# Kernel tuning notes

Hardware: AMD Instinct MI355X
Metric: run time of the kernel (lower is better)

The kernel has to match this reference:

```python
import jax, jax.numpy as jnp
import numpy as np

D_MODEL = 1024
NUM_HEADS = 16
HEAD_DIM = D_MODEL // NUM_HEADS


def setup_inputs() -> dict:
    key = jax.random.key(0)
    ks = jax.random.split(key, 5)
    x = jax.random.normal(ks[0], (2, 2048, D_MODEL), dtype=jnp.float32)
    s = 1.0 / np.sqrt(D_MODEL)
    # nn.Linear weight is [out, in]; y = x @ W.T
    Wq = jax.random.normal(ks[1], (D_MODEL, D_MODEL), dtype=jnp.float32) * s
    Wk = jax.random.normal(ks[2], (D_MODEL, D_MODEL), dtype=jnp.float32) * s
    Wv = jax.random.normal(ks[3], (D_MODEL, D_MODEL), dtype=jnp.float32) * s
    Wo = jax.random.normal(ks[4], (D_MODEL, D_MODEL), dtype=jnp.float32) * s
    return {"x": x, "Wq": Wq, "Wk": Wk, "Wv": Wv, "Wo": Wo}


def reference(x, Wq, Wk, Wv, Wo):
    b, s, d = x.shape
    h, hd = NUM_HEADS, HEAD_DIM
    # projections (Linear: x @ W.T), reshape to [b, h, s, hd]
    def proj(W):
        return (x @ W.T).reshape(b, s, h, hd).transpose(0, 2, 1, 3)
    Q, K, V = proj(Wq), proj(Wk), proj(Wv)
    # NOTE: original scales by 1/sqrt(d_model), not 1/sqrt(head_dim)
    scores = jnp.einsum('bhqd,bhkd->bhqk', Q, K) / jnp.sqrt(jnp.float32(d))
    attn = jax.nn.softmax(scores, axis=-1)
    ctx = jnp.einsum('bhqk,bhkd->bhqd', attn, V)
    ctx = ctx.transpose(0, 2, 1, 3).reshape(b, s, d)
    return ctx @ Wo.T
```

## Files before the change

kernel.cpp:

```cpp
#include <hip/hip_runtime.h>
#include <cstddef>
#include <cstdint>

#define SEQ 2048
#define DM 1024
#define NH 16
#define HD 64

typedef _Float16 f16;
typedef __attribute__((ext_vector_type(8))) _Float16 f16x8;
typedef __attribute__((ext_vector_type(4))) _Float16 f16x4;
typedef __attribute__((ext_vector_type(2))) _Float16 f16x2;
typedef __attribute__((ext_vector_type(4))) float f32x4;

__global__ __launch_bounds__(256) void cast_all(const float* __restrict__ x,
                                                const float* __restrict__ Wq,
                                                const float* __restrict__ Wk,
                                                const float* __restrict__ Wv,
                                                const float* __restrict__ Wo,
                                                f16* __restrict__ dst) {
  const int i = blockIdx.x * 256 + threadIdx.x;
  const float* src;
  int off;
  if (i < 1048576) {
    src = x; off = i;
  } else {
    const int j = i - 1048576;
    const int wsel = j >> 18;
    src = (wsel == 0) ? Wq : (wsel == 1) ? Wk : (wsel == 2) ? Wv : Wo;
    off = j & 262143;
  }
  const float4 v = ((const float4*)src)[off];
  f16x4 o = {(f16)v.x, (f16)v.y, (f16)v.z, (f16)v.w};
  ((f16x4*)dst)[i] = o;
}

__device__ __forceinline__ void gload16(const void* g, void* lds) {
  __builtin_amdgcn_global_load_lds((const __attribute__((address_space(1))) void*)g,
                                   (__attribute__((address_space(3))) void*)lds,
                                   16, 0, 0);
}

__device__ __forceinline__ void gemm_tile_db(const f16* __restrict__ A,
                                             const f16* __restrict__ B,
                                             f16* As0, f16* Bs0,
                                             f16* As1, f16* Bs1,
                                             int K, f32x4 acc[4][4]) {
  const int t = threadIdx.x, lane = t & 63, w = t >> 6;
  const int wm = (w & 1) << 6, wn = (w >> 1) << 6;
  const int srow = lane >> 3, sg = lane & 7;
  const int fr = lane & 15, q = lane >> 4;
  const int scol = (sg ^ srow) << 3;
  auto stg = [&](int k0, f16* As, f16* Bs) {
#pragma unroll
    for (int c = 0; c < 4; ++c) {
      const int row = (w << 5) + (c << 3) + srow;
      gload16(A + (size_t)row * K + k0 + scol, As + (w << 11) + (c << 9));
      gload16(B + (size_t)row * K + k0 + scol, Bs + (w << 11) + (c << 9));
    }
  };
  auto comp = [&](const f16* As, const f16* Bs) {
    f16x8 af[4][2], bf[4][2];
#pragma unroll
    for (int i = 0; i < 4; ++i) {
      const int row = wm + (i << 4) + fr;
#pragma unroll
      for (int kh = 0; kh < 2; ++kh)
        af[i][kh] = *(const f16x8*)(As + row * 64 +
                                    ((((kh << 2) | q) ^ (row & 7)) << 3));
    }
#pragma unroll
    for (int j = 0; j < 4; ++j) {
      const int row = wn + (j << 4) + fr;
#pragma unroll
      for (int kh = 0; kh < 2; ++kh)
        bf[j][kh] = *(const f16x8*)(Bs + row * 64 +
                                    ((((kh << 2) | q) ^ (row & 7)) << 3));
    }
#pragma unroll
    for (int kh = 0; kh < 2; ++kh)
#pragma unroll
      for (int i = 0; i < 4; ++i)
#pragma unroll
        for (int j = 0; j < 4; ++j)
          acc[i][j] = __builtin_amdgcn_mfma_f32_16x16x32_f16(af[i][kh], bf[j][kh],
                                                             acc[i][j], 0, 0, 0);
  };
  stg(0, As0, Bs0);
  for (int k0 = 0; k0 < K; k0 += 128) {
    __syncthreads();
    stg(k0 + 64, As1, Bs1);
    comp(As0, Bs0);
    __syncthreads();
    if (k0 + 128 < K) stg(k0 + 128, As0, Bs0);
    comp(As1, Bs1);
  }
}

#define QSCALE 0.04508422003f
__global__ __launch_bounds__(256) void gemm_qkv(
    const f16* __restrict__ xb, const f16* __restrict__ Wqb,
    const f16* __restrict__ Wkb, const f16* __restrict__ Wvb,
    f16* __restrict__ Qb, f16* __restrict__ Kb, f16* __restrict__ Vtg) {
  __shared__ f16 smem[32768];
  f16* As0 = smem;
  f16* Bs0 = smem + 8192;
  f16* As1 = smem + 16384;
  f16* Bs1 = smem + 24576;
  const int which = blockIdx.x >> 3;
  const int bn = (blockIdx.x & 7) << 7;
  const int bm = blockIdx.y << 7;
  const f16* B = (which == 0) ? Wqb : (which == 1) ? Wkb : Wvb;
  f32x4 acc[4][4] = {};
  gemm_tile_db(xb + (size_t)bm * DM, B + (size_t)bn * DM, As0, Bs0, As1, Bs1,
               DM, acc);
  const int lane = threadIdx.x & 63, w = threadIdx.x >> 6;
  const int wm = (w & 1) << 6, wn = (w >> 1) << 6;
  const int col = lane & 15, q = lane >> 4;
  if (which < 2) {
    f16* C = (which == 0) ? Qb : Kb;
    const float sc = (which == 0) ? QSCALE : 1.0f;
#pragma unroll
    for (int i = 0; i < 4; ++i) {
      const int m = bm + wm + (i << 4) + (q << 2);
#pragma unroll
      for (int j = 0; j < 4; ++j) {
        const int n = bn + wn + (j << 4) + col;
#pragma unroll
        for (int r = 0; r < 4; ++r)
          C[(size_t)(m + r) * DM + n] = (f16)(acc[i][j][r] * sc);
      }
    }
  } else {
    __syncthreads();
#pragma unroll
    for (int i = 0; i < 4; ++i) {
      const int m0 = wm + (i << 4) + (q << 2);
      const int cm = m0 >> 3, sub = (m0 >> 2) & 1;
#pragma unroll
      for (int j = 0; j < 4; ++j) {
        const int nl = wn + (j << 4) + col;
        f16x4 o = {(f16)acc[i][j][0], (f16)acc[i][j][1],
                   (f16)acc[i][j][2], (f16)acc[i][j][3]};
        *(f16x4*)(smem + nl * 128 +
                  ((cm ^ (nl & 15) ^ ((nl >> 4) & 3)) << 3) + (sub << 2)) = o;
      }
    }
    __syncthreads();
    const int b = bm >> 11, sb = bm & 2047;
    const int d = threadIdx.x & 63;
#pragma unroll
    for (int pr = 0; pr < 8; ++pr) {
      const int idx0 = (threadIdx.x >> 6) + (pr << 3);
      const int hh = idx0 >> 5;
      const int s40 = idx0 & 31;
      const int s41 = s40 + 4;
      const int nl = (hh << 6) + d;
      f16x4 va, vb;
      {
        const int cm = s40 >> 1, sub = s40 & 1;
        va = *(const f16x4*)(smem + nl * 128 +
                             ((cm ^ (nl & 15) ^ ((nl >> 4) & 3)) << 3) + (sub << 2));
      }
      {
        const int cm = s41 >> 1, sub = s41 & 1;
        vb = *(const f16x4*)(smem + nl * 128 +
                             ((cm ^ (nl & 15) ^ ((nl >> 4) & 3)) << 3) + (sub << 2));
      }
      const int bh = (b << 4) + (bn >> 6) + hh;
      const int kt = (sb >> 6) + (s40 >> 4);
      const int kc2 = (s40 & 15) >> 3, qd = s40 & 3;
      const f16x8 vv = __builtin_shufflevector(va, vb, 0, 1, 2, 3, 4, 5, 6, 7);
      const size_t flat = ((size_t)bh << 17) + ((size_t)kt << 12) +
                          ((size_t)kc2 << 11) + ((size_t)qd << 9) + ((size_t)d << 3);
      *(f16x8*)(Vtg + flat) = vv;
    }
  }
}

__global__ __launch_bounds__(256) void gemm_out(const f16* __restrict__ Ab,
                                                const f16* __restrict__ Wob,
                                                float* __restrict__ out) {
  __shared__ f16 smem[24576];
  f16* As0 = smem;
  f16* As1 = smem + 8192;
  f16* Bs0 = smem + 16384;
  f16* Bs1 = smem + 20480;
  const int bn = blockIdx.x << 6, bm = blockIdx.y << 7;
  const int t = threadIdx.x, lane = t & 63, w = t >> 6;
  const int srow = lane >> 3, sg = lane & 7;
  const int fr = lane & 15, q = lane >> 4;
  const int scol = (sg ^ srow) << 3;
  const f16* A = Ab + (size_t)bm * DM;
  const f16* B = Wob + (size_t)bn * DM;
  const int wm = w << 5;
  f32x4 acc[2][4] = {};
  auto stg = [&](int k0, f16* As, f16* Bs) {
#pragma unroll
    for (int c = 0; c < 4; ++c) {
      const int row = (w << 5) + (c << 3) + srow;
      gload16(A + (size_t)row * DM + k0 + scol, As + (w << 11) + (c << 9));
    }
#pragma unroll
    for (int c = 0; c < 2; ++c) {
      const int row = (w << 4) + (c << 3) + srow;
      gload16(B + (size_t)row * DM + k0 + scol, Bs + (w << 10) + (c << 9));
    }
  };
  auto comp = [&](const f16* As, const f16* Bs) {
    f16x8 af[2][2], bf[4][2];
#pragma unroll
    for (int i = 0; i < 2; ++i) {
      const int row = wm + (i << 4) + fr;
#pragma unroll
      for (int kh = 0; kh < 2; ++kh)
        af[i][kh] = *(const f16x8*)(As + row * 64 +
                                    ((((kh << 2) | q) ^ (row & 7)) << 3));
    }
#pragma unroll
    for (int j = 0; j < 4; ++j) {
      const int row = (j << 4) + fr;
#pragma unroll
      for (int kh = 0; kh < 2; ++kh)
        bf[j][kh] = *(const f16x8*)(Bs + row * 64 +
                                    ((((kh << 2) | q) ^ (row & 7)) << 3));
    }
#pragma unroll
    for (int kh = 0; kh < 2; ++kh)
#pragma unroll
      for (int i = 0; i < 2; ++i)
#pragma unroll
        for (int j = 0; j < 4; ++j)
          acc[i][j] = __builtin_amdgcn_mfma_f32_16x16x32_f16(af[i][kh], bf[j][kh],
                                                             acc[i][j], 0, 0, 0);
  };
  stg(0, As0, Bs0);
  for (int k0 = 0; k0 < DM; k0 += 128) {
    __syncthreads();
    stg(k0 + 64, As1, Bs1);
    comp(As0, Bs0);
    __syncthreads();
    if (k0 + 128 < DM) stg(k0 + 128, As0, Bs0);
    comp(As1, Bs1);
  }
  const int col = lane & 15;
#pragma unroll
  for (int i = 0; i < 2; ++i) {
    const int m = bm + wm + (i << 4) + (q << 2);
#pragma unroll
    for (int j = 0; j < 4; ++j) {
      const int n = bn + (j << 4) + col;
#pragma unroll
      for (int r = 0; r < 4; ++r)
        out[(size_t)(m + r) * DM + n] = acc[i][j][r];
    }
  }
}

__global__ __launch_bounds__(256, 2) void attn_mfma(const f16* __restrict__ Qb,
                                                    const f16* __restrict__ Kb,
                                                    const f16* __restrict__ Vtg,
                                                    f16* __restrict__ Ctx) {
  __shared__ f16 smem[16384];
  const int t = threadIdx.x, lane = t & 63, w = t >> 6;
  const int fr = lane & 15, quad = lane >> 4;
  const int i = blockIdx.x;
  const int j = i >> 3;
  const int bh = ((i & 7) << 2) + (j >> 4);
  const int qt16 = j & 15;
  const int b = bh >> 4, h = bh & 15;

  const size_t qrow0 = (size_t)b * SEQ + qt16 * 128 + w * 32;

  f16x8 Qf[2][2];
#pragma unroll
  for (int qt = 0; qt < 2; ++qt)
#pragma unroll
    for (int hf = 0; hf < 2; ++hf)
      Qf[qt][hf] = *(const f16x8*)(Qb + (qrow0 + qt * 16 + fr) * DM + h * HD +
                                   hf * 32 + (quad << 3));

  const int krow = lane >> 2;
  const int kkc = ((lane & 3) - (lane >> 3)) & 3;
  const f16* Kg = Kb + ((size_t)b * SEQ + 16 * w + krow) * DM + h * HD + (kkc << 3);
  const f16* Vg = Vtg + ((size_t)bh << 17) + (((w << 7) + lane) << 3);

  const int crd = ((fr >> 1) << 3) | ((fr & 1) << 2) | (((fr >> 1) + quad) & 3);

  f16* K0 = smem;
  f16* K1 = smem + 4096;
  f16* V0 = smem + 8192;
  f16* V1 = smem + 12288;

  auto stage = [&](int kt, f16* Kimg, f16* Vimg) {
#pragma unroll
    for (int hf = 0; hf < 2; ++hf)
      gload16(Kg + (size_t)kt * 64 * DM + hf * 32, Kimg + (hf << 11) + (w << 9));
#pragma unroll
    for (int c = 0; c < 2; ++c)
      gload16(Vg + kt * 4096 + (c << 9), Vimg + (w << 10) + (c << 9));
  };

  f32x4 acc[2][4] = {};
  float lacc[2] = {0.f, 0.f};
  f16x8 Kf[4][2];
  f16x8 VfA[4][2], pfA[2][2];
  f16x8 VfB[4][2], pfB[2][2];

  auto frags = [&](const f16* KR, const f16* VR, f16x8 (&Vf)[4][2]) {
#pragma unroll
    for (int mt = 0; mt < 4; ++mt)
#pragma unroll
      for (int hf = 0; hf < 2; ++hf)
        Kf[mt][hf] = *(const f16x8*)(KR + (crd << 3) + (hf << 11) + (mt << 9));
#pragma unroll
    for (int dt = 0; dt < 4; ++dt)
#pragma unroll
      for (int kc = 0; kc < 2; ++kc)
        Vf[dt][kc] = *(const f16x8*)(VR + (kc << 11) + (quad << 9) +
                                     (((dt << 4) | fr) << 3));
  };

  auto qkexp = [&](f16x8 (&pf)[2][2]) {
    f32x4 z[2][4] = {};
    __builtin_amdgcn_s_setprio(1);
#pragma unroll
    for (int hf = 0; hf < 2; ++hf)
#pragma unroll
      for (int qt = 0; qt < 2; ++qt)
#pragma unroll
        for (int mt = 0; mt < 4; ++mt)
          z[qt][mt] = __builtin_amdgcn_mfma_f32_16x16x32_f16(Kf[mt][hf], Qf[qt][hf],
                                                             z[qt][mt], 0, 0, 0);
    __builtin_amdgcn_s_setprio(0);
#pragma unroll
    for (int qt = 0; qt < 2; ++qt) {
      f16x4 p4[4];
#pragma unroll
      for (int mt = 0; mt < 4; ++mt) {
        const float p0 = __builtin_amdgcn_exp2f(z[qt][mt][0]);
        const float p1 = __builtin_amdgcn_exp2f(z[qt][mt][1]);
        const float p2 = __builtin_amdgcn_exp2f(z[qt][mt][2]);
        const float p3 = __builtin_amdgcn_exp2f(z[qt][mt][3]);
        lacc[qt] += (p0 + p1) + (p2 + p3);
        const f16x2 lo = __builtin_bit_cast(f16x2, __builtin_amdgcn_cvt_pkrtz(p0, p1));
        const f16x2 hi = __builtin_bit_cast(f16x2, __builtin_amdgcn_cvt_pkrtz(p2, p3));
        f16x4 pv4; pv4.x = lo.x; pv4.y = lo.y; pv4.z = hi.x; pv4.w = hi.y;
        p4[mt] = pv4;
      }
      pf[qt][0] = __builtin_shufflevector(p4[0], p4[1], 0, 1, 2, 3, 4, 5, 6, 7);
      pf[qt][1] = __builtin_shufflevector(p4[2], p4[3], 0, 1, 2, 3, 4, 5, 6, 7);
    }
  };

  auto pv = [&](const f16x8 (&Vf)[4][2], const f16x8 (&pf)[2][2]) {
    __builtin_amdgcn_s_setprio(1);
#pragma unroll
    for (int kc = 0; kc < 2; ++kc)
#pragma unroll
      for (int dt = 0; dt < 4; ++dt)
#pragma unroll
        for (int qt = 0; qt < 2; ++qt)
          acc[qt][dt] = __builtin_amdgcn_mfma_f32_16x16x32_f16(Vf[dt][kc], pf[qt][kc],
                                                               acc[qt][dt], 0, 0, 0);
    __builtin_amdgcn_s_setprio(0);
  };

  stage(0, K0, V0);

  __syncthreads();
  stage(1, K1, V1);
  frags(K0, V0, VfA);
  qkexp(pfA);
  __syncthreads();
  stage(2, K0, V0);
  frags(K1, V1, VfB);
  qkexp(pfB);

  for (int kt = 2; kt < 30; kt += 2) {
    __syncthreads();
    stage(kt + 1, K1, V1);
    pv(VfA, pfA);
    frags(K0, V0, VfA);
    qkexp(pfA);
    __syncthreads();
    stage(kt + 2, K0, V0);
    pv(VfB, pfB);
    frags(K1, V1, VfB);
    qkexp(pfB);
  }

  __syncthreads();
  stage(31, K1, V1);
  pv(VfA, pfA);
  frags(K0, V0, VfA);
  qkexp(pfA);
  __syncthreads();
  pv(VfB, pfB);
  frags(K1, V1, VfB);
  qkexp(pfB);
  pv(VfA, pfA);
  pv(VfB, pfB);

  float inv[2];
#pragma unroll
  for (int qt = 0; qt < 2; ++qt) {
    float l = lacc[qt];
    l += __shfl_xor(l, 16);
    l += __shfl_xor(l, 32);
    inv[qt] = __builtin_amdgcn_rcpf(l);
  }

  __syncthreads();
  f16* T = smem + (w << 11);
#pragma unroll
  for (int qt = 0; qt < 2; ++qt)
#pragma unroll
    for (int dt = 0; dt < 4; ++dt) {
      f16x4 o = {(f16)(acc[qt][dt][0] * inv[qt]), (f16)(acc[qt][dt][1] * inv[qt]),
                 (f16)(acc[qt][dt][2] * inv[qt]), (f16)(acc[qt][dt][3] * inv[qt])};
      *(f16x4*)(T + (qt * 16 + fr) * 64 + dt * 16 + (quad << 2)) = o;
    }
#pragma unroll
  for (int p = 0; p < 4; ++p) {
    const int ql = p * 8 + (lane >> 3);
    const f16x8 v = *(const f16x8*)(T + ql * 64 + ((lane & 7) << 3));
    *(f16x8*)(Ctx + (qrow0 + ql) * DM + h * HD + ((lane & 7) << 3)) = v;
  }
}

extern "C" void kernel_launch(void* const* d_in, const int* in_sizes, int n_in,
                              void* d_out, int out_size, void* d_ws, size_t ws_size,
                              hipStream_t stream) {
  const float* x  = (const float*)d_in[0];
  const float* Wq = (const float*)d_in[1];
  const float* Wk = (const float*)d_in[2];
  const float* Wv = (const float*)d_in[3];
  const float* Wo = (const float*)d_in[4];

  char* ws = (char*)d_ws;
  f16* xb  = (f16*)(ws);
  f16* Wb  = (f16*)(ws + (8u << 20));
  f16* Wqb = Wb;
  f16* Wkb = Wb + 1048576;
  f16* Wvb = Wb + 2097152;
  f16* Wob = Wb + 3145728;
  f16* Qb  = (f16*)(ws + (16u << 20));
  f16* Kb  = (f16*)(ws + (24u << 20));
  f16* Vtg = (f16*)(ws + (32u << 20));
  f16* Ctx = (f16*)(ws + (40u << 20));

  cast_all<<<8192, 256, 0, stream>>>(x, Wq, Wk, Wv, Wo, xb);

  gemm_qkv<<<dim3(24, 32), 256, 0, stream>>>(xb, Wqb, Wkb, Wvb, Qb, Kb, Vtg);
  attn_mfma<<<dim3(2 * NH * (SEQ / 128)), 256, 0, stream>>>(Qb, Kb, Vtg, Ctx);
  gemm_out<<<dim3(16, 32), 256, 0, stream>>>(Ctx, Wob, (float*)d_out);
}
```

Measured before the change: 164.6 us.

## Enlarge QKV projection GEMM tile to 256x256 with 512-thread blocks

```diff
diff --git a/kernel.cpp b/kernel.cpp
--- a/kernel.cpp
+++ b/kernel.cpp
@@ -41,91 +41,82 @@
                                    16, 0, 0);
 }
 
-__device__ __forceinline__ void gemm_tile_db(const f16* __restrict__ A,
-                                             const f16* __restrict__ B,
-                                             f16* As0, f16* Bs0,
-                                             f16* As1, f16* Bs1,
-                                             int K, f32x4 acc[4][4]) {
+#define QSCALE 0.04508422003f
+__global__ __launch_bounds__(512) void gemm_qkv(
+    const f16* __restrict__ xb, const f16* __restrict__ Wqb,
+    const f16* __restrict__ Wkb, const f16* __restrict__ Wvb,
+    f16* __restrict__ Qb, f16* __restrict__ Kb, f16* __restrict__ Vtg) {
+  __shared__ f16 smem[65536];
+  f16* As0 = smem;
+  f16* Bs0 = smem + 16384;
+  f16* As1 = smem + 32768;
+  f16* Bs1 = smem + 49152;
+  const int which = blockIdx.x >> 2;
+  const int bn = blockIdx.x & 3;
+  const int bm = blockIdx.y;
+  const f16* B = (which == 0) ? Wqb : (which == 1) ? Wkb : Wvb;
+  const f16* A = xb + ((size_t)bm << 8) * DM;
+  const f16* Bt = B + ((size_t)bn << 8) * DM;
+
   const int t = threadIdx.x, lane = t & 63, w = t >> 6;
-  const int wm = (w & 1) << 6, wn = (w >> 1) << 6;
+  const int wm = (w & 1) << 7, wn = (w >> 1) << 6;
   const int srow = lane >> 3, sg = lane & 7;
   const int fr = lane & 15, q = lane >> 4;
   const int scol = (sg ^ srow) << 3;
+
+  f32x4 acc[8][4] = {};
+
   auto stg = [&](int k0, f16* As, f16* Bs) {
 #pragma unroll
     for (int c = 0; c < 4; ++c) {
       const int row = (w << 5) + (c << 3) + srow;
-      gload16(A + (size_t)row * K + k0 + scol, As + (w << 11) + (c << 9));
-      gload16(B + (size_t)row * K + k0 + scol, Bs + (w << 11) + (c << 9));
+      gload16(A + (size_t)row * DM + k0 + scol, As + (w << 11) + (c << 9));
+      gload16(Bt + (size_t)row * DM + k0 + scol, Bs + (w << 11) + (c << 9));
     }
   };
   auto comp = [&](const f16* As, const f16* Bs) {
-    f16x8 af[4][2], bf[4][2];
-#pragma unroll
-    for (int i = 0; i < 4; ++i) {
-      const int row = wm + (i << 4) + fr;
-#pragma unroll
-      for (int kh = 0; kh < 2; ++kh)
-        af[i][kh] = *(const f16x8*)(As + row * 64 +
-                                    ((((kh << 2) | q) ^ (row & 7)) << 3));
-    }
-#pragma unroll
-    for (int j = 0; j < 4; ++j) {
-      const int row = wn + (j << 4) + fr;
-#pragma unroll
-      for (int kh = 0; kh < 2; ++kh)
-        bf[j][kh] = *(const f16x8*)(Bs + row * 64 +
-                                    ((((kh << 2) | q) ^ (row & 7)) << 3));
-    }
-#pragma unroll
-    for (int kh = 0; kh < 2; ++kh)
-#pragma unroll
-      for (int i = 0; i < 4; ++i)
+#pragma unroll
+    for (int kh = 0; kh < 2; ++kh) {
+      f16x8 bfk[4];
+#pragma unroll
+      for (int j = 0; j < 4; ++j) {
+        const int rowb = wn + (j << 4) + fr;
+        bfk[j] = *(const f16x8*)(Bs + rowb * 64 +
+                                 ((((kh << 2) | q) ^ (rowb & 7)) << 3));
+      }
+#pragma unroll
+      for (int i = 0; i < 8; ++i) {
+        const int rowa = wm + (i << 4) + fr;
+        const f16x8 a = *(const f16x8*)(As + rowa * 64 +
+                                        ((((kh << 2) | q) ^ (rowa & 7)) << 3));
 #pragma unroll
         for (int j = 0; j < 4; ++j)
-          acc[i][j] = __builtin_amdgcn_mfma_f32_16x16x32_f16(af[i][kh], bf[j][kh],
+          acc[i][j] = __builtin_amdgcn_mfma_f32_16x16x32_f16(a, bfk[j],
                                                              acc[i][j], 0, 0, 0);
-  };
+      }
+    }
+  };
+
   stg(0, As0, Bs0);
-  for (int k0 = 0; k0 < K; k0 += 128) {
+  for (int k0 = 0; k0 < DM; k0 += 128) {
     __syncthreads();
     stg(k0 + 64, As1, Bs1);
     comp(As0, Bs0);
     __syncthreads();
-    if (k0 + 128 < K) stg(k0 + 128, As0, Bs0);
+    if (k0 + 128 < DM) stg(k0 + 128, As0, Bs0);
     comp(As1, Bs1);
   }
-}
-
-#define QSCALE 0.04508422003f
-__global__ __launch_bounds__(256) void gemm_qkv(
-    const f16* __restrict__ xb, const f16* __restrict__ Wqb,
-    const f16* __restrict__ Wkb, const f16* __restrict__ Wvb,
-    f16* __restrict__ Qb, f16* __restrict__ Kb, f16* __restrict__ Vtg) {
-  __shared__ f16 smem[32768];
-  f16* As0 = smem;
-  f16* Bs0 = smem + 8192;
-  f16* As1 = smem + 16384;
-  f16* Bs1 = smem + 24576;
-  const int which = blockIdx.x >> 3;
-  const int bn = (blockIdx.x & 7) << 7;
-  const int bm = blockIdx.y << 7;
-  const f16* B = (which == 0) ? Wqb : (which == 1) ? Wkb : Wvb;
-  f32x4 acc[4][4] = {};
-  gemm_tile_db(xb + (size_t)bm * DM, B + (size_t)bn * DM, As0, Bs0, As1, Bs1,
-               DM, acc);
-  const int lane = threadIdx.x & 63, w = threadIdx.x >> 6;
-  const int wm = (w & 1) << 6, wn = (w >> 1) << 6;
-  const int col = lane & 15, q = lane >> 4;
+
+  const int col = lane & 15;
   if (which < 2) {
     f16* C = (which == 0) ? Qb : Kb;
     const float sc = (which == 0) ? QSCALE : 1.0f;
 #pragma unroll
-    for (int i = 0; i < 4; ++i) {
-      const int m = bm + wm + (i << 4) + (q << 2);
+    for (int i = 0; i < 8; ++i) {
+      const int m = (bm << 8) + wm + (i << 4) + (q << 2);
 #pragma unroll
       for (int j = 0; j < 4; ++j) {
-        const int n = bn + wn + (j << 4) + col;
+        const int n = (bn << 8) + wn + (j << 4) + col;
 #pragma unroll
         for (int r = 0; r < 4; ++r)
           C[(size_t)(m + r) * DM + n] = (f16)(acc[i][j][r] * sc);
@@ -134,42 +125,32 @@
   } else {
     __syncthreads();
 #pragma unroll
-    for (int i = 0; i < 4; ++i) {
-      const int m0 = wm + (i << 4) + (q << 2);
-      const int cm = m0 >> 3, sub = (m0 >> 2) & 1;
+    for (int i = 0; i < 8; ++i) {
+      const int m4b = (wm >> 2) + (i << 2) + q;
 #pragma unroll
       for (int j = 0; j < 4; ++j) {
         const int nl = wn + (j << 4) + col;
         f16x4 o = {(f16)acc[i][j][0], (f16)acc[i][j][1],
                    (f16)acc[i][j][2], (f16)acc[i][j][3]};
-        *(f16x4*)(smem + nl * 128 +
-                  ((cm ^ (nl & 15) ^ ((nl >> 4) & 3)) << 3) + (sub << 2)) = o;
+        *(f16x4*)(smem + nl * 256 + ((m4b ^ ((nl & 15) << 2)) << 2)) = o;
       }
     }
     __syncthreads();
-    const int b = bm >> 11, sb = bm & 2047;
-    const int d = threadIdx.x & 63;
-#pragma unroll
-    for (int pr = 0; pr < 8; ++pr) {
-      const int idx0 = (threadIdx.x >> 6) + (pr << 3);
-      const int hh = idx0 >> 5;
-      const int s40 = idx0 & 31;
+    const int b = bm >> 3;
+    const int d = t & 63;
+#pragma unroll
+    for (int pr = 0; pr < 16; ++pr) {
+      const int idx = (t >> 6) + (pr << 3);
+      const int hh = idx >> 5, p5 = idx & 31;
+      const int s40 = ((p5 >> 2) << 3) | (p5 & 3);
       const int s41 = s40 + 4;
       const int nl = (hh << 6) + d;
-      f16x4 va, vb;
-      {
-        const int cm = s40 >> 1, sub = s40 & 1;
-        va = *(const f16x4*)(smem + nl * 128 +
-                             ((cm ^ (nl & 15) ^ ((nl >> 4) & 3)) << 3) + (sub << 2));
-      }
-      {
-        const int cm = s41 >> 1, sub = s41 & 1;
-        vb = *(const f16x4*)(smem + nl * 128 +
-                             ((cm ^ (nl & 15) ^ ((nl >> 4) & 3)) << 3) + (sub << 2));
-      }
-      const int bh = (b << 4) + (bn >> 6) + hh;
-      const int kt = (sb >> 6) + (s40 >> 4);
-      const int kc2 = (s40 & 15) >> 3, qd = s40 & 3;
+      const int sw = (nl & 15) << 2;
+      const f16x4 va = *(const f16x4*)(smem + nl * 256 + ((s40 ^ sw) << 2));
+      const f16x4 vb = *(const f16x4*)(smem + nl * 256 + ((s41 ^ sw) << 2));
+      const int bh = (b << 4) + (bn << 2) + hh;
+      const int kt = ((bm & 7) << 2) + (s40 >> 4);
+      const int kc2 = (s40 >> 3) & 1, qd = s40 & 3;
       const f16x8 vv = __builtin_shufflevector(va, vb, 0, 1, 2, 3, 4, 5, 6, 7);
       const size_t flat = ((size_t)bh << 17) + ((size_t)kt << 12) +
                           ((size_t)kc2 << 11) + ((size_t)qd << 9) + ((size_t)d << 3);
@@ -452,7 +433,7 @@
 
   cast_all<<<8192, 256, 0, stream>>>(x, Wq, Wk, Wv, Wo, xb);
 
-  gemm_qkv<<<dim3(24, 32), 256, 0, stream>>>(xb, Wqb, Wkb, Wvb, Qb, Kb, Vtg);
+  gemm_qkv<<<dim3(12, 16), 512, 0, stream>>>(xb, Wqb, Wkb, Wvb, Qb, Kb, Vtg);
   attn_mfma<<<dim3(2 * NH * (SEQ / 128)), 256, 0, stream>>>(Qb, Kb, Vtg, Ctx);
   gemm_out<<<dim3(16, 32), 256, 0, stream>>>(Ctx, Wob, (float*)d_out);
 }
```

New measurement: 179.3 us. 8.9% more time.
